# Optimization experiments

Measured on AMD Instinct MI355X. Metric: run time of the kernel, lower is better.

Reference implementation:

```python
import jax, jax.numpy as jnp
import numpy as np
import math

EMBED_DIM = 1024
NUM_HEADS = 16
NUM_KV_HEADS = 16
DEPTH = 12
HEAD_DIM = EMBED_DIM // NUM_HEADS // 2  # 32
LAMBDA_INIT = 0.8 - 0.6 * math.exp(-0.3 * DEPTH)
EPS = 1e-5
THETA = 0.0001


def rope(q):
    # q: (b, s, h, d) with interleaved pairs, matches apply_rotary_pos_emb
    b, s, h, d = q.shape
    pos = jnp.arange(s, dtype=jnp.float32)[:, None]                      # (s,1)
    freq = 1.0 / (THETA ** (2.0 * jnp.arange(d // 2, dtype=jnp.float32) / d))
    ang = pos * freq                                                     # (s, d/2)
    cos = jnp.cos(ang)[None, :, None, :].astype(q.dtype)
    sin = jnp.sin(ang)[None, :, None, :].astype(q.dtype)
    qr = q.reshape(b, s, h, d // 2, 2)
    q0, q1 = qr[..., 0], qr[..., 1]
    out = jnp.stack([q0 * cos - q1 * sin, q0 * sin + q1 * cos], axis=-1)
    return out.reshape(q.shape)


def setup_inputs() -> dict:
    key = jax.random.key(0)
    ks = jax.random.split(key, 10)
    d = EMBED_DIM
    sd = 1.0 / math.sqrt(d)
    return {
        "x": jax.random.normal(ks[0], (1, 2048, d), dtype=jnp.float32),
        "Wq": jax.random.normal(ks[1], (d, d), dtype=jnp.float32) * sd,
        "Wk": jax.random.normal(ks[2], (d, d), dtype=jnp.float32) * sd,
        "Wv": jax.random.normal(ks[3], (d, d), dtype=jnp.float32) * sd,
        "Wo": jax.random.normal(ks[4], (d, d), dtype=jnp.float32) * sd,
        "lambda_q1": jax.random.normal(ks[5], (HEAD_DIM,), dtype=jnp.float32) * 0.1,
        "lambda_k1": jax.random.normal(ks[6], (HEAD_DIM,), dtype=jnp.float32) * 0.1,
        "lambda_q2": jax.random.normal(ks[7], (HEAD_DIM,), dtype=jnp.float32) * 0.1,
        "lambda_k2": jax.random.normal(ks[8], (HEAD_DIM,), dtype=jnp.float32) * 0.1,
        "subln_g": jnp.ones((2 * HEAD_DIM,), dtype=jnp.float32),
    }


def reference(x, Wq, Wk, Wv, Wo, lambda_q1, lambda_k1, lambda_q2, lambda_k2, subln_g):
    b, s, d = x.shape
    H, hd = NUM_HEADS, HEAD_DIM
    scaling = hd ** (-0.5)

    q = (x @ Wq).reshape(b, s, 2 * H, hd)
    k = (x @ Wk).reshape(b, s, 2 * NUM_KV_HEADS, hd)
    v = (x @ Wv).reshape(b, s, NUM_KV_HEADS, 2 * hd)

    q = rope(q).transpose(0, 2, 1, 3) * scaling   # (b, 2H, s, hd)
    k = rope(k).transpose(0, 2, 1, 3)             # (b, 2H, s, hd)  (n_rep = 1)
    v = v.transpose(0, 2, 1, 3)                   # (b, H, s, 2hd)

    scores = jnp.einsum("bhqd,bhkd->bhqk", q, k)  # (b, 2H, s, s)
    probs = jax.nn.softmax(scores.astype(jnp.float32), axis=-1).astype(scores.dtype)

    lam1 = jnp.exp(jnp.sum(lambda_q1 * lambda_k1))
    lam2 = jnp.exp(jnp.sum(lambda_q2 * lambda_k2))
    lam = (lam1 - lam2 + LAMBDA_INIT).astype(q.dtype)

    probs = probs.reshape(b, H, 2, s, s)
    w = probs[:, :, 0] - lam * probs[:, :, 1]     # (b, H, s, s)

    attn = jnp.einsum("bhqk,bhkd->bhqd", w, v)    # (b, H, s, 2hd)
    rms = jax.lax.rsqrt(jnp.mean(attn * attn, axis=-1, keepdims=True) + EPS)
    attn = attn * rms * subln_g
    attn = attn * (1.0 - LAMBDA_INIT)

    attn = attn.transpose(0, 2, 1, 3).reshape(b, s, H * 2 * hd)
    return attn @ Wo
```

## Files before the change

kernel.cpp:

```cpp
#include <hip/hip_runtime.h>
#include <math.h>

#define S 2048
#define D 1024
#define NH 16
#define HD 32
#define HD2 64

static constexpr float SCALE_Q_EXP2  = 0.17677669529663687f * 1.4426950408889634f;
static constexpr float LAMBDA_INIT_F = 0.78360576653162450f;
static constexpr float ONE_MINUS_LI  = 0.21639423346837553f;

typedef unsigned short u16;
typedef unsigned int   u32;
typedef __attribute__((ext_vector_type(4)))  unsigned short u16x4;
typedef __attribute__((ext_vector_type(8)))  short          bfrag;
typedef __attribute__((ext_vector_type(16))) float          f16acc;
typedef __attribute__((ext_vector_type(4)))  unsigned int   uint4v;

__device__ __forceinline__ u16 f2bf(float f) {
    u32 u = __builtin_bit_cast(u32, f);
    return (u16)((u + 0x7FFFu + ((u >> 16) & 1u)) >> 16);
}
__device__ __forceinline__ f16acc fillv(float v) {
    f16acc z;
#pragma unroll
    for (int i = 0; i < 16; ++i) z[i] = v;
    return z;
}
__device__ __forceinline__ float exp2_raw(float x) {
#if __has_builtin(__builtin_amdgcn_exp2f)
    return __builtin_amdgcn_exp2f(x);
#else
    float r;
    asm volatile("v_exp_f32 %0, %1\n\ts_nop 1" : "=v"(r) : "v"(x));
    return r;
#endif
}
#define MFMA(a, b, c) __builtin_amdgcn_mfma_f32_32x32x16_bf16(a, b, c, 0, 0, 0)

__device__ __forceinline__ void gload16(const u16* src, u16* lds) {
    __builtin_amdgcn_global_load_lds((const __attribute__((address_space(1))) void*)src,
                                     (__attribute__((address_space(3))) void*)lds, 16, 0, 0);
}

__global__ void prep_kernel(const float* __restrict__ lq1, const float* __restrict__ lk1,
                            const float* __restrict__ lq2, const float* __restrict__ lk2,
                            float* __restrict__ cosT, float* __restrict__ sinT,
                            float* __restrict__ lamOut) {
    int idx = blockIdx.x * blockDim.x + threadIdx.x;
    if (idx < S * 16) {
        int p = idx >> 4;
        int m = idx & 15;
        const double base = (double)1.0e-4f;
        float pf   = (float)pow(base, (double)m * (1.0 / 16.0));
        float freq = 1.0f / pf;
        float angf = (float)p * freq;
        double a = (double)angf;
        cosT[idx] = (float)cos(a);
        sinT[idx] = (float)sin(a);
    }
    if (blockIdx.x == 0 && threadIdx.x == 0) {
        float s1 = 0.f, s2 = 0.f;
        for (int i = 0; i < HD; ++i) {
            s1 += lq1[i] * lk1[i];
            s2 += lq2[i] * lk2[i];
        }
        *lamOut = expf(s1) - expf(s2) + LAMBDA_INIT_F;
    }
}

__global__ __launch_bounds__(256)
void convert_kernel(const float* __restrict__ x,  const float* __restrict__ Wq,
                    const float* __restrict__ Wk, const float* __restrict__ Wv,
                    const float* __restrict__ Wo,
                    u16* __restrict__ xb,  u16* __restrict__ WqT, u16* __restrict__ WkT,
                    u16* __restrict__ WvT, u16* __restrict__ WoT) {
    const int z = blockIdx.y;
    if (z == 0) {
        const int i = blockIdx.x * 256 + threadIdx.x;
        const float4 v = *(const float4*)&x[(size_t)i * 4];
        u16x4 r; r.x = f2bf(v.x); r.y = f2bf(v.y); r.z = f2bf(v.z); r.w = f2bf(v.w);
        *(u16x4*)&xb[(size_t)i * 4] = r;
        return;
    }
    const int b = blockIdx.x;
    if (b >= 256) return;
    __shared__ u16 Ts[64][66];
    const float* W = (z == 1) ? Wq : (z == 2) ? Wk : (z == 3) ? Wv : Wo;
    u16* T = (z == 1) ? WqT : (z == 2) ? WkT : (z == 3) ? WvT : WoT;
    const int k0 = (b >> 4) * 64, n0 = (b & 15) * 64;
    const int rg = threadIdx.x >> 4, cc = (threadIdx.x & 15) * 4;
#pragma unroll
    for (int i = 0; i < 4; ++i) {
        const int r = rg * 4 + i;
        const float4 v = *(const float4*)&W[(size_t)(k0 + r) * D + n0 + cc];
        Ts[r][cc + 0] = f2bf(v.x); Ts[r][cc + 1] = f2bf(v.y);
        Ts[r][cc + 2] = f2bf(v.z); Ts[r][cc + 3] = f2bf(v.w);
    }
    __syncthreads();
#pragma unroll
    for (int i = 0; i < 4; ++i) {
        const int rn = rg * 4 + i;
        u16x4 res;
        res.x = Ts[cc + 0][rn]; res.y = Ts[cc + 1][rn];
        res.z = Ts[cc + 2][rn]; res.w = Ts[cc + 3][rn];
        *(u16x4*)&T[(size_t)(n0 + rn) * D + k0 + cc] = res;
    }
}

template<int MODE>
__global__ __launch_bounds__(256)
void mm_kernel(const u16* __restrict__ Ab, const u16* __restrict__ B0,
               const u16* __restrict__ B1, const u16* __restrict__ B2,
               const float* __restrict__ cosT, const float* __restrict__ sinT,
               u16* __restrict__ Qb, u16* __restrict__ Kb, u16* __restrict__ VT,
               float* __restrict__ Of) {
    __shared__ u16 As[128 * 32];
    __shared__ u16 Bs[128 * 32];

    const int nb   = blockIdx.x;
    const int row0 = blockIdx.y * 128;
    const int tid  = threadIdx.x;
    const int wave = tid >> 6;
    const int lane = tid & 63;
    const int ql   = lane & 31;
    const int hi   = lane >> 5;
    const int wr   = wave >> 1;
    const int wc   = wave & 1;

    const u16* Bt;
    int col0B;
    if (MODE == 0) {
        Bt = (nb < 8) ? B0 : (nb < 16) ? B1 : B2;
        col0B = (nb & 7) * 128;
    } else {
        Bt = B0;
        col0B = nb * 128;
    }

    const int rIn  = lane >> 2;
    const int kof  = 8 * (lane & 3);
    const size_t aRow0 = (size_t)(row0 + 16 * wave       + rIn) * D + kof;
    const size_t aRow1 = (size_t)(row0 + 16 * (wave + 4) + rIn) * D + kof;
    const size_t bRow0 = (size_t)(col0B + 16 * wave       + rIn) * D + kof;
    const size_t bRow1 = (size_t)(col0B + 16 * (wave + 4) + rIn) * D + kof;
    u16* ldsA0 = &As[512 * wave + 8 * lane];
    u16* ldsA1 = &As[512 * (wave + 4) + 8 * lane];
    u16* ldsB0 = &Bs[512 * wave + 8 * lane];
    u16* ldsB1 = &Bs[512 * (wave + 4) + 8 * lane];

    const int aoff = (wr * 64 + ql) * 32 + hi * 8;
    const int boff = (wc * 64 + ql) * 32 + hi * 8;

    f16acc acc00 = fillv(0.f), acc01 = fillv(0.f), acc10 = fillv(0.f), acc11 = fillv(0.f);

    for (int kk = 0; kk < D; kk += 32) {
        gload16(Ab + aRow0 + kk, ldsA0);
        gload16(Ab + aRow1 + kk, ldsA1);
        gload16(Bt + bRow0 + kk, ldsB0);
        gload16(Bt + bRow1 + kk, ldsB1);
        __syncthreads();
#pragma unroll
        for (int ks = 0; ks < 2; ++ks) {
            const bfrag a0 = *(const bfrag*)&As[aoff + ks * 16];
            const bfrag a1 = *(const bfrag*)&As[aoff + 32 * 32 + ks * 16];
            const bfrag b0 = *(const bfrag*)&Bs[boff + ks * 16];
            const bfrag b1 = *(const bfrag*)&Bs[boff + 32 * 32 + ks * 16];
            acc00 = MFMA(a0, b0, acc00);
            acc01 = MFMA(a0, b1, acc01);
            acc10 = MFMA(a1, b0, acc10);
            acc11 = MFMA(a1, b1, acc11);
        }
        __syncthreads();
    }

    f16acc accA[2][2];
    accA[0][0] = acc00; accA[0][1] = acc01; accA[1][0] = acc10; accA[1][1] = acc11;

    if (MODE == 0 && nb < 16) {
        u16* Dst = (nb < 8) ? Qb : Kb;
        const float sc = (nb < 8) ? SCALE_Q_EXP2 : 1.0f;
        const int m = ql >> 1;
        const bool ev = (ql & 1) == 0;
#pragma unroll
        for (int i = 0; i < 2; ++i)
#pragma unroll
        for (int j = 0; j < 2; ++j) {
            const int n = (nb & 7) * 128 + wc * 64 + j * 32 + ql;
            const int head = n >> 5;
            u16* hb = Dst + (size_t)head * S * HD;
#pragma unroll
            for (int r = 0; r < 16; ++r) {
                const int row = row0 + wr * 64 + i * 32 + 4 * hi + (r & 3) + 8 * (r >> 2);
                const float self = accA[i][j][r];
                const float part = __shfl_xor(self, 1);
                const float c = cosT[(row << 4) + m], s = sinT[(row << 4) + m];
                const float res = ev ? (self * c - part * s) : (part * s + self * c);
                hb[(size_t)row * HD + ql] = f2bf(res * sc);
            }
        }
    } else if (MODE == 0) {
#pragma unroll
        for (int i = 0; i < 2; ++i)
#pragma unroll
        for (int j = 0; j < 2; ++j) {
            const int n = (nb & 7) * 128 + wc * 64 + j * 32 + ql;
            const int head = n >> 6, d = n & 63;
            u16* tb = VT + (size_t)head * 131072;
#pragma unroll
            for (int q = 0; q < 4; ++q) {
                const int row = row0 + wr * 64 + i * 32 + 4 * hi + 8 * q;
                const int off = (d * 32 + (row & 31)) ^ ((d & 3) << 3);
                u16x4 res;
                res.x = f2bf(accA[i][j][4 * q + 0]);
                res.y = f2bf(accA[i][j][4 * q + 1]);
                res.z = f2bf(accA[i][j][4 * q + 2]);
                res.w = f2bf(accA[i][j][4 * q + 3]);
                *(u16x4*)&tb[(size_t)(row >> 5) * 2048 + off] = res;
            }
        }
    } else {
#pragma unroll
        for (int i = 0; i < 2; ++i)
#pragma unroll
        for (int j = 0; j < 2; ++j) {
            const int gcol = col0B + wc * 64 + j * 32 + ql;
#pragma unroll
            for (int r = 0; r < 16; ++r) {
                const int row = row0 + wr * 64 + i * 32 + 4 * hi + (r & 3) + 8 * (r >> 2);
                Of[(size_t)row * D + gcol] = accA[i][j][r];
            }
        }
    }
}

__global__ __launch_bounds__(512, 2)
void attn_mfma(const u16* __restrict__ Qb, const u16* __restrict__ Kb,
               const u16* __restrict__ Vt2, const float* __restrict__ lamPtr,
               const float* __restrict__ g, u16* __restrict__ AO) {
    const int h    = blockIdx.y;
    const int tid  = threadIdx.x;
    const int wave = tid >> 6;
    const int lane = tid & 63;
    const int hi   = lane >> 5;
    const int ql   = lane & 31;
    const int t    = wave >> 2;
    const int wv   = wave & 3;
    const int q0   = (blockIdx.x * 2 + t) * 32;
    const int cbase = wv * 16;

    __shared__ float CMB[2][64][66];

    const u16* qp1 = Qb + ((size_t)(2 * h) * S + q0 + ql) * HD + 8 * hi;
    const u16* qp2 = qp1 + (size_t)S * HD;
    bfrag qf1[2], qf2[2];
    qf1[0] = *(const bfrag*)(qp1);      qf1[1] = *(const bfrag*)(qp1 + 16);
    qf2[0] = *(const bfrag*)(qp2);      qf2[1] = *(const bfrag*)(qp2 + 16);

    const u16* kp1 = Kb + ((size_t)(2 * h) * S + ql) * HD + 8 * hi;
    const u16* kp2 = kp1 + (size_t)S * HD;
    const u16* vchunk = Vt2 + (size_t)h * 131072;

    int roff[2][2];
#pragma unroll
    for (int dt = 0; dt < 2; ++dt)
#pragma unroll
        for (int s = 0; s < 2; ++s) {
            const int d = dt * 32 + ql;
            roff[dt][s] = d * 32 + (((2 * s + hi) ^ (d & 3)) << 3);
        }

    const f16acc ZR = fillv(0.f);
    uint4v ou; ou[0] = ou[1] = ou[2] = ou[3] = 0x3F803F80u;
    const bfrag ONES = __builtin_bit_cast(bfrag, ou);

    f16acc acc1[2], acc2[2];
    acc1[0] = fillv(0.f); acc1[1] = fillv(0.f);
    acc2[0] = fillv(0.f); acc2[1] = fillv(0.f);
    float l1 = 0.f, l2 = 0.f;

    bfrag kA1[2], kA2[2], kB1[2], kB2[2];
    bfrag vA[2][2], vB[2][2];
    kA1[0] = *(const bfrag*)(kp1 + (size_t)cbase * 1024);
    kA1[1] = *(const bfrag*)(kp1 + (size_t)cbase * 1024 + 16);
    kA2[0] = *(const bfrag*)(kp2 + (size_t)cbase * 1024);
    kA2[1] = *(const bfrag*)(kp2 + (size_t)cbase * 1024 + 16);
#pragma unroll
    for (int s = 0; s < 2; ++s)
#pragma unroll
        for (int dt = 0; dt < 2; ++dt)
            vA[s][dt] = *(const bfrag*)(vchunk + (size_t)cbase * 2048 + roff[dt][s]);

    auto body = [&](bfrag (&kc1)[2], bfrag (&kc2)[2], bfrag (&vc)[2][2],
                    bfrag (&kn1)[2], bfrag (&kn2)[2], bfrag (&vn)[2][2], int cn) {
        kn1[0] = *(const bfrag*)(kp1 + (size_t)cn * 1024);
        kn1[1] = *(const bfrag*)(kp1 + (size_t)cn * 1024 + 16);
        kn2[0] = *(const bfrag*)(kp2 + (size_t)cn * 1024);
        kn2[1] = *(const bfrag*)(kp2 + (size_t)cn * 1024 + 16);
#pragma unroll
        for (int s = 0; s < 2; ++s)
#pragma unroll
            for (int dt = 0; dt < 2; ++dt)
                vn[s][dt] = *(const bfrag*)(vchunk + (size_t)cn * 2048 + roff[dt][s]);

        __builtin_amdgcn_s_setprio(1);
        f16acc s1 = MFMA(kc1[0], qf1[0], ZR);  s1 = MFMA(kc1[1], qf1[1], s1);
        f16acc s2 = MFMA(kc2[0], qf2[0], ZR);  s2 = MFMA(kc2[1], qf2[1], s2);
        __builtin_amdgcn_s_setprio(0);

#pragma unroll
        for (int r = 0; r < 16; ++r) {
            s1[r] = exp2_raw(s1[r]);
            s2[r] = exp2_raw(s2[r]);
        }

        u32 w1[8], w2[8];
#pragma unroll
        for (int j = 0; j < 8; ++j) {
            asm("v_cvt_pk_bf16_f32 %0, %1, %2" : "=v"(w1[j]) : "v"(s1[2 * j]), "v"(s1[2 * j + 1]));
            asm("v_cvt_pk_bf16_f32 %0, %1, %2" : "=v"(w2[j]) : "v"(s2[2 * j]), "v"(s2[2 * j + 1]));
        }
        asm("v_permlane32_swap_b32 %0, %1" : "+v"(w1[0]), "+v"(w1[2]));
        asm("v_permlane32_swap_b32 %0, %1" : "+v"(w1[1]), "+v"(w1[3]));
        asm("v_permlane32_swap_b32 %0, %1" : "+v"(w1[4]), "+v"(w1[6]));
        asm("v_permlane32_swap_b32 %0, %1" : "+v"(w1[5]), "+v"(w1[7]));
        asm("v_permlane32_swap_b32 %0, %1" : "+v"(w2[0]), "+v"(w2[2]));
        asm("v_permlane32_swap_b32 %0, %1" : "+v"(w2[1]), "+v"(w2[3]));
        asm("v_permlane32_swap_b32 %0, %1" : "+v"(w2[4]), "+v"(w2[6]));
        asm("v_permlane32_swap_b32 %0, %1" : "+v"(w2[5]), "+v"(w2[7]));
        uint4v u;
        bfrag p1[2], p2[2];
        u[0] = w1[0]; u[1] = w1[1]; u[2] = w1[2]; u[3] = w1[3];
        p1[0] = __builtin_bit_cast(bfrag, u);
        u[0] = w1[4]; u[1] = w1[5]; u[2] = w1[6]; u[3] = w1[7];
        p1[1] = __builtin_bit_cast(bfrag, u);
        u[0] = w2[0]; u[1] = w2[1]; u[2] = w2[2]; u[3] = w2[3];
        p2[0] = __builtin_bit_cast(bfrag, u);
        u[0] = w2[4]; u[1] = w2[5]; u[2] = w2[6]; u[3] = w2[7];
        p2[1] = __builtin_bit_cast(bfrag, u);

        __builtin_amdgcn_s_setprio(1);
        acc1[0] = MFMA(vc[0][0], p1[0], acc1[0]);
        acc1[0] = MFMA(vc[1][0], p1[1], acc1[0]);
        acc1[1] = MFMA(vc[0][1], p1[0], acc1[1]);
        acc1[1] = MFMA(vc[1][1], p1[1], acc1[1]);
        acc2[0] = MFMA(vc[0][0], p2[0], acc2[0]);
        acc2[0] = MFMA(vc[1][0], p2[1], acc2[0]);
        acc2[1] = MFMA(vc[0][1], p2[0], acc2[1]);
        acc2[1] = MFMA(vc[1][1], p2[1], acc2[1]);
        f16acc t1 = MFMA(ONES, p1[0], ZR);  t1 = MFMA(ONES, p1[1], t1);
        f16acc t2 = MFMA(ONES, p2[0], ZR);  t2 = MFMA(ONES, p2[1], t2);
        __builtin_amdgcn_s_setprio(0);
        l1 += t1[0];
        l2 += t2[0];
    };

    for (int i = 0; i < 16; i += 2) {
        const int c0 = cbase + i;
        body(kA1, kA2, vA, kB1, kB2, vB, c0 + 1);
        const int c2 = (i + 2 < 16) ? c0 + 2 : c0 + 1;
        body(kB1, kB2, vB, kA1, kA2, vA, c2);
    }

#pragma unroll 1
    for (int p = 1; p < 4; ++p) {
        if (wv == p) {
            float* c0 = &CMB[t][lane][0];
#pragma unroll
            for (int dt = 0; dt < 2; ++dt)
#pragma unroll
                for (int r = 0; r < 16; ++r) {
                    c0[dt * 16 + r]      = acc1[dt][r];
                    c0[32 + dt * 16 + r] = acc2[dt][r];
                }
            c0[64] = l1; c0[65] = l2;
        }
        __syncthreads();
        if (wv == 0) {
            const float* c0 = &CMB[t][lane][0];
#pragma unroll
            for (int dt = 0; dt < 2; ++dt)
#pragma unroll
                for (int r = 0; r < 16; ++r) {
                    acc1[dt][r] += c0[dt * 16 + r];
                    acc2[dt][r] += c0[32 + dt * 16 + r];
                }
            l1 += c0[64]; l2 += c0[65];
        }
        __syncthreads();
    }

    if (wv == 0) {
        const float lam = *lamPtr;
        const float inv1 = 1.0f / l1, inv2 = 1.0f / l2;
        float o_[2][16];
        float ss = 0.f;
#pragma unroll
        for (int dt = 0; dt < 2; ++dt)
#pragma unroll
            for (int r = 0; r < 16; ++r) {
                float o = acc1[dt][r] * inv1 - lam * (acc2[dt][r] * inv2);
                o_[dt][r] = o;
                ss += o * o;
            }
        ss += __shfl_xor(ss, 32);
        const float rs = rsqrtf(ss * (1.0f / 64.0f) + 1e-5f);

        u16* aorow = AO + (size_t)(q0 + ql) * D + h * 64;
#pragma unroll
        for (int dt = 0; dt < 2; ++dt)
#pragma unroll
            for (int G = 0; G < 4; ++G) {
                const int dbase = dt * 32 + G * 8 + hi * 4;
                const float4 gv = *(const float4*)&g[dbase];
                u16x4 res;
                res.x = f2bf(o_[dt][4 * G + 0] * rs * gv.x * ONE_MINUS_LI);
                res.y = f2bf(o_[dt][4 * G + 1] * rs * gv.y * ONE_MINUS_LI);
                res.z = f2bf(o_[dt][4 * G + 2] * rs * gv.z * ONE_MINUS_LI);
                res.w = f2bf(o_[dt][4 * G + 3] * rs * gv.w * ONE_MINUS_LI);
                *(u16x4*)&aorow[dbase] = res;
            }
    }
}

extern "C" void kernel_launch(void* const* d_in, const int* in_sizes, int n_in,
                              void* d_out, int out_size, void* d_ws, size_t ws_size,
                              hipStream_t stream) {
    const float* x   = (const float*)d_in[0];
    const float* Wq  = (const float*)d_in[1];
    const float* Wk  = (const float*)d_in[2];
    const float* Wv  = (const float*)d_in[3];
    const float* Wo  = (const float*)d_in[4];
    const float* lq1 = (const float*)d_in[5];
    const float* lk1 = (const float*)d_in[6];
    const float* lq2 = (const float*)d_in[7];
    const float* lk2 = (const float*)d_in[8];
    const float* g   = (const float*)d_in[9];
    float* out = (float*)d_out;

    char* ws = (char*)d_ws;
    float* cosT = (float*)(ws);
    float* sinT = (float*)(ws + 131072);
    float* lam  = (float*)(ws + 262144);
    char*  b    = ws + 262400;
    u16*   Qb   = (u16*)(b);
    u16*   Kb   = (u16*)(b + 4194304);
    u16*   VT   = (u16*)(b + 8388608);
    u16*   AO   = (u16*)(b + 12582912);
    u16*   xb   = (u16*)(b + 16777216);
    u16*   WqT  = (u16*)(b + 20971520);
    u16*   WkT  = (u16*)(b + 23068672);
    u16*   WvT  = (u16*)(b + 25165824);
    u16*   WoT  = (u16*)(b + 27262976);

    prep_kernel<<<128, 256, 0, stream>>>(lq1, lk1, lq2, lk2, cosT, sinT, lam);
    convert_kernel<<<dim3(2048, 5), 256, 0, stream>>>(x, Wq, Wk, Wv, Wo,
                                                      xb, WqT, WkT, WvT, WoT);

    mm_kernel<0><<<dim3(24, 16), 256, 0, stream>>>(xb, WqT, WkT, WvT, cosT, sinT,
                                                   Qb, Kb, VT, nullptr);

    attn_mfma<<<dim3(32, NH), 512, 0, stream>>>(Qb, Kb, VT, lam, g, AO);

    mm_kernel<1><<<dim3(8, 16), 256, 0, stream>>>(AO, WoT, nullptr, nullptr, cosT, sinT,
                                                  nullptr, nullptr, nullptr, out);
}
```

Before: 110.3 us.

## Stage K/V chunks through double-buffered LDS shared by both query tiles

The attention kernel now copies K and V chunks into a double-buffered shared-memory area, with one wave group loading K and the other loading V. Both query-tile groups in the block then read from that shared copy instead of each issuing its own global loads into registers. The QKV projection epilogue writes K in a chunked, XOR-swizzled layout so the LDS reads avoid bank conflicts, and the combine buffer now aliases the staging area. This halves global K/V traffic per block and adds a block-wide barrier on every iteration, which may cost more in stalls than the saved loads.

```diff
diff --git a/kernel.cpp b/kernel.cpp
--- a/kernel.cpp
+++ b/kernel.cpp
@@ -114,7 +114,7 @@
 void mm_kernel(const u16* __restrict__ Ab, const u16* __restrict__ B0,
                const u16* __restrict__ B1, const u16* __restrict__ B2,
                const float* __restrict__ cosT, const float* __restrict__ sinT,
-               u16* __restrict__ Qb, u16* __restrict__ Kb, u16* __restrict__ VT,
+               u16* __restrict__ Qb, u16* __restrict__ Kb2, u16* __restrict__ VT,
                float* __restrict__ Of) {
     __shared__ u16 As[128 * 32];
     __shared__ u16 Bs[128 * 32];
@@ -178,9 +178,7 @@
     f16acc accA[2][2];
     accA[0][0] = acc00; accA[0][1] = acc01; accA[1][0] = acc10; accA[1][1] = acc11;
 
-    if (MODE == 0 && nb < 16) {
-        u16* Dst = (nb < 8) ? Qb : Kb;
-        const float sc = (nb < 8) ? SCALE_Q_EXP2 : 1.0f;
+    if (MODE == 0 && nb < 8) {
         const int m = ql >> 1;
         const bool ev = (ql & 1) == 0;
 #pragma unroll
@@ -189,7 +187,7 @@
         for (int j = 0; j < 2; ++j) {
             const int n = (nb & 7) * 128 + wc * 64 + j * 32 + ql;
             const int head = n >> 5;
-            u16* hb = Dst + (size_t)head * S * HD;
+            u16* hb = Qb + (size_t)head * S * HD;
 #pragma unroll
             for (int r = 0; r < 16; ++r) {
                 const int row = row0 + wr * 64 + i * 32 + 4 * hi + (r & 3) + 8 * (r >> 2);
@@ -197,7 +195,29 @@
                 const float part = __shfl_xor(self, 1);
                 const float c = cosT[(row << 4) + m], s = sinT[(row << 4) + m];
                 const float res = ev ? (self * c - part * s) : (part * s + self * c);
-                hb[(size_t)row * HD + ql] = f2bf(res * sc);
+                hb[(size_t)row * HD + ql] = f2bf(res * SCALE_Q_EXP2);
+            }
+        }
+    } else if (MODE == 0 && nb < 16) {
+        const int m = ql >> 1;
+        const bool ev = (ql & 1) == 0;
+#pragma unroll
+        for (int i = 0; i < 2; ++i)
+#pragma unroll
+        for (int j = 0; j < 2; ++j) {
+            const int n = (nb & 7) * 128 + wc * 64 + j * 32 + ql;
+            const int h2 = n >> 5;
+            u16* hb = Kb2 + (size_t)h2 * 65536;
+#pragma unroll
+            for (int r = 0; r < 16; ++r) {
+                const int row = row0 + wr * 64 + i * 32 + 4 * hi + (r & 3) + 8 * (r >> 2);
+                const float self = accA[i][j][r];
+                const float part = __shfl_xor(self, 1);
+                const float c = cosT[(row << 4) + m], s = sinT[(row << 4) + m];
+                const float res = ev ? (self * c - part * s) : (part * s + self * c);
+                const int idx = (row >> 5) * 1024 + (row & 31) * 32
+                              + (((ql >> 3) ^ (row & 3)) << 3) + (ql & 7);
+                hb[idx] = f2bf(res);
             }
         }
     } else if (MODE == 0) {
@@ -236,7 +256,7 @@
 }
 
 __global__ __launch_bounds__(512, 2)
-void attn_mfma(const u16* __restrict__ Qb, const u16* __restrict__ Kb,
+void attn_mfma(const u16* __restrict__ Qb, const u16* __restrict__ Kb2,
                const u16* __restrict__ Vt2, const float* __restrict__ lamPtr,
                const float* __restrict__ g, u16* __restrict__ AO) {
     const int h    = blockIdx.y;
@@ -250,7 +270,8 @@
     const int q0   = (blockIdx.x * 2 + t) * 32;
     const int cbase = wv * 16;
 
-    __shared__ float CMB[2][64][66];
+    __shared__ __align__(16) u16 KV[2][4][4096];
+    float (*CMB)[64][66] = (float(*)[64][66])&KV[0][0][0];
 
     const u16* qp1 = Qb + ((size_t)(2 * h) * S + q0 + ql) * HD + 8 * hi;
     const u16* qp2 = qp1 + (size_t)S * HD;
@@ -258,18 +279,13 @@
     qf1[0] = *(const bfrag*)(qp1);      qf1[1] = *(const bfrag*)(qp1 + 16);
     qf2[0] = *(const bfrag*)(qp2);      qf2[1] = *(const bfrag*)(qp2 + 16);
 
-    const u16* kp1 = Kb + ((size_t)(2 * h) * S + ql) * HD + 8 * hi;
-    const u16* kp2 = kp1 + (size_t)S * HD;
-    const u16* vchunk = Vt2 + (size_t)h * 131072;
-
-    int roff[2][2];
-#pragma unroll
-    for (int dt = 0; dt < 2; ++dt)
-#pragma unroll
-        for (int s = 0; s < 2; ++s) {
-            const int d = dt * 32 + ql;
-            roff[dt][s] = d * 32 + (((2 * s + hi) ^ (d & 3)) << 3);
-        }
+    const u16* k1g = Kb2 + (size_t)(2 * h) * 65536;
+    const u16* k2g = k1g + 65536;
+    const u16* vg  = Vt2 + (size_t)h * 131072;
+
+    int pofs[2];
+#pragma unroll
+    for (int s = 0; s < 2; ++s) pofs[s] = (((2 * s + hi) ^ (ql & 3)) << 3);
 
     const f16acc ZR = fillv(0.f);
     uint4v ou; ou[0] = ou[1] = ou[2] = ou[3] = 0x3F803F80u;
@@ -280,29 +296,41 @@
     acc2[0] = fillv(0.f); acc2[1] = fillv(0.f);
     float l1 = 0.f, l2 = 0.f;
 
-    bfrag kA1[2], kA2[2], kB1[2], kB2[2];
-    bfrag vA[2][2], vB[2][2];
-    kA1[0] = *(const bfrag*)(kp1 + (size_t)cbase * 1024);
-    kA1[1] = *(const bfrag*)(kp1 + (size_t)cbase * 1024 + 16);
-    kA2[0] = *(const bfrag*)(kp2 + (size_t)cbase * 1024);
-    kA2[1] = *(const bfrag*)(kp2 + (size_t)cbase * 1024 + 16);
-#pragma unroll
-    for (int s = 0; s < 2; ++s)
-#pragma unroll
-        for (int dt = 0; dt < 2; ++dt)
-            vA[s][dt] = *(const bfrag*)(vchunk + (size_t)cbase * 2048 + roff[dt][s]);
-
-    auto body = [&](bfrag (&kc1)[2], bfrag (&kc2)[2], bfrag (&vc)[2][2],
-                    bfrag (&kn1)[2], bfrag (&kn2)[2], bfrag (&vn)[2][2], int cn) {
-        kn1[0] = *(const bfrag*)(kp1 + (size_t)cn * 1024);
-        kn1[1] = *(const bfrag*)(kp1 + (size_t)cn * 1024 + 16);
-        kn2[0] = *(const bfrag*)(kp2 + (size_t)cn * 1024);
-        kn2[1] = *(const bfrag*)(kp2 + (size_t)cn * 1024 + 16);
-#pragma unroll
-        for (int s = 0; s < 2; ++s)
+    auto stage = [&](int buf, int c) {
+        u16* base = &KV[buf][wv][0];
+        if (t == 0) {
+            const u16* k1 = k1g + (size_t)c * 1024;
+            const u16* k2 = k2g + (size_t)c * 1024;
+            gload16(k1 + lane * 8,       base + lane * 8);
+            gload16(k1 + 512 + lane * 8, base + 512 + lane * 8);
+            gload16(k2 + lane * 8,       base + 1024 + lane * 8);
+            gload16(k2 + 512 + lane * 8, base + 1536 + lane * 8);
+        } else {
+            const u16* vv = vg + (size_t)c * 2048;
+            gload16(vv + lane * 8,        base + 2048 + lane * 8);
+            gload16(vv + 512 + lane * 8,  base + 2560 + lane * 8);
+            gload16(vv + 1024 + lane * 8, base + 3072 + lane * 8);
+            gload16(vv + 1536 + lane * 8, base + 3584 + lane * 8);
+        }
+    };
+
+    stage(0, cbase);
+    __syncthreads();
+    int cur = 0;
+
+    for (int i = 0; i < 16; ++i) {
+        if (i < 15) stage(cur ^ 1, cbase + i + 1);
+
+        const u16* Kq = &KV[cur][wv][0];
+        bfrag kc1[2], kc2[2], vc[2][2];
+#pragma unroll
+        for (int s = 0; s < 2; ++s) {
+            kc1[s] = *(const bfrag*)(Kq + ql * 32 + pofs[s]);
+            kc2[s] = *(const bfrag*)(Kq + 1024 + ql * 32 + pofs[s]);
 #pragma unroll
             for (int dt = 0; dt < 2; ++dt)
-                vn[s][dt] = *(const bfrag*)(vchunk + (size_t)cn * 2048 + roff[dt][s]);
+                vc[s][dt] = *(const bfrag*)(Kq + 2048 + (dt * 32 + ql) * 32 + pofs[s]);
+        }
 
         __builtin_amdgcn_s_setprio(1);
         f16acc s1 = MFMA(kc1[0], qf1[0], ZR);  s1 = MFMA(kc1[1], qf1[1], s1);
@@ -354,13 +382,9 @@
         __builtin_amdgcn_s_setprio(0);
         l1 += t1[0];
         l2 += t2[0];
-    };
-
-    for (int i = 0; i < 16; i += 2) {
-        const int c0 = cbase + i;
-        body(kA1, kA2, vA, kB1, kB2, vB, c0 + 1);
-        const int c2 = (i + 2 < 16) ? c0 + 2 : c0 + 1;
-        body(kB1, kB2, vB, kA1, kA2, vA, c2);
+
+        __syncthreads();
+        cur ^= 1;
     }
 
 #pragma unroll 1
@@ -445,7 +469,7 @@
     float* lam  = (float*)(ws + 262144);
     char*  b    = ws + 262400;
     u16*   Qb   = (u16*)(b);
-    u16*   Kb   = (u16*)(b + 4194304);
+    u16*   Kb2  = (u16*)(b + 4194304);
     u16*   VT   = (u16*)(b + 8388608);
     u16*   AO   = (u16*)(b + 12582912);
     u16*   xb   = (u16*)(b + 16777216);
@@ -459,9 +483,9 @@
                                                       xb, WqT, WkT, WvT, WoT);
 
     mm_kernel<0><<<dim3(24, 16), 256, 0, stream>>>(xb, WqT, WkT, WvT, cosT, sinT,
-                                                   Qb, Kb, VT, nullptr);
-
-    attn_mfma<<<dim3(32, NH), 512, 0, stream>>>(Qb, Kb, VT, lam, g, AO);
+                                                   Qb, Kb2, VT, nullptr);
+
+    attn_mfma<<<dim3(32, NH), 512, 0, stream>>>(Qb, Kb2, VT, lam, g, AO);
 
     mm_kernel<1><<<dim3(8, 16), 256, 0, stream>>>(AO, WoT, nullptr, nullptr, cosT, sinT,
                                                   nullptr, nullptr, nullptr, out);
```

Result: slower. 117.1 us (+6.2%).
